# Kernel optimization log

Measured on AMD Instinct MI355X. Metric: run time of the kernel, lower is better.

Reference implementation:

```python
import jax, jax.numpy as jnp
import numpy as np

DIM = 512
HEADS = 8
DIM_HEAD = 64
LANDMARKS = 256
PINV_ITERS = 6
RES_K = 33


def layernorm(x, g, b, eps=1e-5):
    mu = jnp.mean(x, -1, keepdims=True)
    var = jnp.mean((x - mu) ** 2, -1, keepdims=True)
    return (x - mu) / jnp.sqrt(var + eps) * g + b


def moore_penrose_pinv(x, iters=PINV_ITERS):
    abs_x = jnp.abs(x)
    col = abs_x.sum(-1)
    row = abs_x.sum(-2)
    z = jnp.swapaxes(x, -1, -2) / (jnp.max(col) * jnp.max(row))
    I = jnp.eye(x.shape[-1], dtype=x.dtype)
    for _ in range(iters):
        xz = x @ z
        z = 0.25 * z @ (13.0 * I - xz @ (15.0 * I - xz @ (7.0 * I - xz)))
    return z


def nystrom_attention(x, Wqkv, Wout, bout, res_w):
    b, n, _ = x.shape
    m = LANDMARKS
    pad = (m - n % m) % m
    if pad:
        x = jnp.pad(x, ((0, 0), (pad, 0), (0, 0)))  # front pad, as in lucidrains impl
    qkv = x @ Wqkv  # (b, np, 3*inner)
    q, k, v = jnp.split(qkv, 3, axis=-1)
    to_heads = lambda t: t.reshape(b, -1, HEADS, DIM_HEAD).transpose(0, 2, 1, 3)
    q, k, v = to_heads(q), to_heads(k), to_heads(v)  # (b,h,np,d)
    q = q * (DIM_HEAD ** -0.5)
    l = -(-n // m)  # ceil(n/m), tokens per landmark
    ql = q.reshape(b, HEADS, m, l, DIM_HEAD).sum(3) / l  # (b,h,m,d)
    kl = k.reshape(b, HEADS, m, l, DIM_HEAD).sum(3) / l
    sim1 = jnp.einsum('bhid,bhjd->bhij', q, kl)   # (b,h,np,m)
    sim2 = jnp.einsum('bhid,bhjd->bhij', ql, kl)  # (b,h,m,m)
    sim3 = jnp.einsum('bhid,bhjd->bhij', ql, k)   # (b,h,m,np)
    a1 = jax.nn.softmax(sim1, -1)
    a2 = jax.nn.softmax(sim2, -1)
    a3 = jax.nn.softmax(sim3, -1)
    a2_inv = moore_penrose_pinv(a2)
    out = (a1 @ a2_inv) @ (a3 @ v)  # (b,h,np,d)
    # depthwise residual conv along sequence (kernel 33x1, groups=heads, no bias)
    res = jax.lax.conv_general_dilated(
        v, res_w, (1, 1), [(RES_K // 2, RES_K // 2), (0, 0)],
        dimension_numbers=('NCHW', 'OIHW', 'NCHW'), feature_group_count=HEADS)
    out = out + res
    out = out.transpose(0, 2, 1, 3).reshape(b, -1, HEADS * DIM_HEAD)
    out = out @ Wout + bout
    return out[:, -n:]


def depthwise2d(x, w, b, pad):
    y = jax.lax.conv_general_dilated(
        x, w, (1, 1), [(pad, pad), (pad, pad)],
        dimension_numbers=('NCHW', 'OIHW', 'NCHW'), feature_group_count=DIM)
    return y + b[None, :, None, None]


def ppeg(x, H, W, w7, b7, w5, b5, w3, b3):
    B, _, C = x.shape
    cls_tok, feat = x[:, :1], x[:, 1:]
    cnn = feat.transpose(0, 2, 1).reshape(B, C, H, W)
    y = depthwise2d(cnn, w7, b7, 3) + cnn + depthwise2d(cnn, w5, b5, 2) + depthwise2d(cnn, w3, b3, 1)
    y = y.reshape(B, C, H * W).transpose(0, 2, 1)
    return jnp.concatenate([cls_tok, y], axis=1)


def setup_inputs() -> dict:
    key = jax.random.key(0)
    ks = jax.random.split(key, 20)
    s = 0.02
    n_classes = 5
    inp = {
        'data': jax.random.normal(ks[0], (1, 15000, 1024), jnp.float32),
        'W_fc1': jax.random.normal(ks[1], (1024, DIM), jnp.float32) * s,
        'b_fc1': jnp.zeros((DIM,), jnp.float32),
        'cls_token': jax.random.normal(ks[2], (1, 1, DIM), jnp.float32),
        'ln1_g': jnp.ones((DIM,), jnp.float32), 'ln1_b': jnp.zeros((DIM,), jnp.float32),
        'qkv1': jax.random.normal(ks[3], (DIM, 3 * HEADS * DIM_HEAD), jnp.float32) * s,
        'out1_w': jax.random.normal(ks[4], (HEADS * DIM_HEAD, DIM), jnp.float32) * s,
        'out1_b': jnp.zeros((DIM,), jnp.float32),
        'res1': jax.random.normal(ks[5], (HEADS, 1, RES_K, 1), jnp.float32) * s,
        'w7': jax.random.normal(ks[6], (DIM, 1, 7, 7), jnp.float32) * s,
        'b7': jnp.zeros((DIM,), jnp.float32),
        'w5': jax.random.normal(ks[7], (DIM, 1, 5, 5), jnp.float32) * s,
        'b5': jnp.zeros((DIM,), jnp.float32),
        'w3': jax.random.normal(ks[8], (DIM, 1, 3, 3), jnp.float32) * s,
        'b3': jnp.zeros((DIM,), jnp.float32),
        'ln2_g': jnp.ones((DIM,), jnp.float32), 'ln2_b': jnp.zeros((DIM,), jnp.float32),
        'qkv2': jax.random.normal(ks[9], (DIM, 3 * HEADS * DIM_HEAD), jnp.float32) * s,
        'out2_w': jax.random.normal(ks[10], (HEADS * DIM_HEAD, DIM), jnp.float32) * s,
        'out2_b': jnp.zeros((DIM,), jnp.float32),
        'res2': jax.random.normal(ks[11], (HEADS, 1, RES_K, 1), jnp.float32) * s,
        'norm_g': jnp.ones((DIM,), jnp.float32), 'norm_b': jnp.zeros((DIM,), jnp.float32),
        'W_fc2': jax.random.normal(ks[12], (DIM, n_classes), jnp.float32) * s,
        'b_fc2': jnp.zeros((n_classes,), jnp.float32),
    }
    return inp


def reference(data, W_fc1, b_fc1, cls_token, ln1_g, ln1_b, qkv1, out1_w, out1_b, res1,
              w7, b7, w5, b5, w3, b3, ln2_g, ln2_b, qkv2, out2_w, out2_b, res2,
              norm_g, norm_b, W_fc2, b_fc2):
    h = jax.nn.relu(data @ W_fc1 + b_fc1)  # (B, N, 512)
    N = h.shape[1]
    _H = int(np.ceil(np.sqrt(N)))
    _W = _H
    add = _H * _W - N
    h = jnp.concatenate([h, h[:, :add]], axis=1)  # pad to square grid
    B = h.shape[0]
    h = jnp.concatenate([jnp.broadcast_to(cls_token, (B, 1, DIM)), h], axis=1)
    h = h + nystrom_attention(layernorm(h, ln1_g, ln1_b), qkv1, out1_w, out1_b, res1)
    h = ppeg(h, _H, _W, w7, b7, w5, b5, w3, b3)
    h = h + nystrom_attention(layernorm(h, ln2_g, ln2_b), qkv2, out2_w, out2_b, res2)
    h = layernorm(h, norm_g, norm_b)[:, 0]
    logits = h @ W_fc2 + b_fc2
    Y_prob = jax.nn.softmax(logits, -1)
    Y_hat = jnp.argmax(logits, -1)
    return logits, Y_prob, Y_hat
```

## Files before the change

kernel.cpp:

```cpp
#include <hip/hip_runtime.h>
#include <math.h>

#define NP 15360
#define NPQ 15488
#define NTOK 15130
#define HG 123

typedef __attribute__((ext_vector_type(8))) short s8b;
typedef __attribute__((ext_vector_type(4))) float f4;

__device__ inline float bf2f(ushort u) { return __uint_as_float(((unsigned)u) << 16); }
__device__ inline ushort f2bf(float f) {
    unsigned u = __float_as_uint(f);
    unsigned r = (u + 0x7fffu + ((u >> 16) & 1u)) >> 16;
    return (ushort)r;
}

__global__ __launch_bounds__(256)
void gemm_f32(const float* __restrict__ A, int lda, long sA,
              const float* __restrict__ B, int ldb, long sB,
              float* __restrict__ C, int ldc, long sC,
              int M, int N, int K,
              const float* __restrict__ bias,
              const float* __restrict__ E, int ldE, long sE, float eS,
              float cS, int relu, int accum)
{
    A += (long)blockIdx.z * sA;
    B += (long)blockIdx.z * sB;
    C += (long)blockIdx.z * sC;
    if (E) E += (long)blockIdx.z * sE;
    const int m0 = blockIdx.y * 64, n0 = blockIdx.x * 64;
    const int t = threadIdx.x;
    const int tx = t & 15, ty = t >> 4;
    __shared__ float As[16][64];
    __shared__ float Bs[16][64];
    float acc[4][4] = {};
    const int arow = t >> 2, akc = (t & 3) * 4;
    const int brow = t >> 4, bnc = (t & 15) * 4;
    for (int k0 = 0; k0 < K; k0 += 16) {
        float4 av = make_float4(0.f, 0.f, 0.f, 0.f);
        if (m0 + arow < M) av = *(const float4*)(A + (long)(m0 + arow) * lda + k0 + akc);
        As[akc + 0][arow] = av.x; As[akc + 1][arow] = av.y;
        As[akc + 2][arow] = av.z; As[akc + 3][arow] = av.w;
        float4 bv = *(const float4*)(B + (long)(k0 + brow) * ldb + n0 + bnc);
        *(float4*)&Bs[brow][bnc] = bv;
        __syncthreads();
#pragma unroll
        for (int kk = 0; kk < 16; ++kk) {
            float4 a4 = *(const float4*)&As[kk][ty * 4];
            float4 b4 = *(const float4*)&Bs[kk][tx * 4];
            float a[4] = {a4.x, a4.y, a4.z, a4.w};
            float b[4] = {b4.x, b4.y, b4.z, b4.w};
#pragma unroll
            for (int i = 0; i < 4; i++)
#pragma unroll
                for (int j = 0; j < 4; j++) acc[i][j] = fmaf(a[i], b[j], acc[i][j]);
        }
        __syncthreads();
    }
#pragma unroll
    for (int i = 0; i < 4; i++) {
        int m = m0 + ty * 4 + i;
        if (m < M) {
#pragma unroll
            for (int j = 0; j < 4; j++) {
                int n = n0 + tx * 4 + j;
                float v = cS * acc[i][j];
                if (E) v = fmaf(eS, E[(long)m * ldE + n], v);
                if (bias) v += bias[n];
                if (relu) v = fmaxf(v, 0.f);
                if (accum) C[(long)m * ldc + n] += v;
                else C[(long)m * ldc + n] = v;
            }
        }
    }
}

template<int MT, int NT, int WROWS, int WCOLS>
__global__ __launch_bounds__(256)
void gemm_mfma(const ushort* __restrict__ A, int lda, long sA,
               const ushort* __restrict__ Bt, int ldb, long sB,
               float* __restrict__ C, int ldc, long sC,
               int M, int K,
               const float* __restrict__ bias, int relu, int accum)
{
    constexpr int TM = MT * 16 * WROWS;
    constexpr int TN = NT * 16 * WCOLS;
    constexpr int BKP = 40;
    __shared__ ushort As[TM * BKP];
    __shared__ ushort Bs[TN * BKP];
    A  += (long)blockIdx.z * sA;
    Bt += (long)blockIdx.z * sB;
    C  += (long)blockIdx.z * sC;
    const int t = threadIdx.x;
    const int m0 = blockIdx.y * TM, n0 = blockIdx.x * TN;
    const int w = t >> 6, l = t & 63;
    const int wm = (w / WCOLS) * (MT * 16), wn = (w % WCOLS) * (NT * 16);
    const int lr = l & 15;
    const int lk = (l >> 4) * 8;
    f4 acc[MT][NT] = {};
    for (int k0 = 0; k0 < K; k0 += 32) {
        for (int c = t; c < TM * 4; c += 256) {
            int row = c >> 2, kc = (c & 3) * 8;
            s8b v = *(const s8b*)(A + (long)(m0 + row) * lda + k0 + kc);
            *(s8b*)(&As[row * BKP + kc]) = v;
        }
        for (int c = t; c < TN * 4; c += 256) {
            int row = c >> 2, kc = (c & 3) * 8;
            s8b v = *(const s8b*)(Bt + (long)(n0 + row) * ldb + k0 + kc);
            *(s8b*)(&Bs[row * BKP + kc]) = v;
        }
        __syncthreads();
        s8b af[MT], bf[NT];
#pragma unroll
        for (int i = 0; i < MT; i++) af[i] = *(const s8b*)(&As[(wm + i * 16 + lr) * BKP + lk]);
#pragma unroll
        for (int j = 0; j < NT; j++) bf[j] = *(const s8b*)(&Bs[(wn + j * 16 + lr) * BKP + lk]);
#pragma unroll
        for (int i = 0; i < MT; i++)
#pragma unroll
            for (int j = 0; j < NT; j++)
                acc[i][j] = __builtin_amdgcn_mfma_f32_16x16x32_bf16(af[i], bf[j], acc[i][j], 0, 0, 0);
        __syncthreads();
    }
    const int orow = (l >> 4) * 4;
#pragma unroll
    for (int i = 0; i < MT; i++) {
#pragma unroll
        for (int r = 0; r < 4; r++) {
            int m = m0 + wm + i * 16 + orow + r;
            if (m < M) {
#pragma unroll
                for (int j = 0; j < NT; j++) {
                    int n = n0 + wn + j * 16 + lr;
                    float vv = acc[i][j][r];
                    if (bias) vv += bias[n];
                    if (relu) vv = fmaxf(vv, 0.f);
                    if (accum) C[(long)m * ldc + n] += vv;
                    else C[(long)m * ldc + n] = vv;
                }
            }
        }
    }
}

__global__ __launch_bounds__(256)
void gemm_nn16(const ushort* __restrict__ A, const ushort* __restrict__ B,
               const ushort* __restrict__ E, ushort* __restrict__ C,
               int N, int K, float cS, float eS, long sAB)
{
    __shared__ ushort As[64 * 40];
    __shared__ ushort Bs[64 * 40];
    A += (long)blockIdx.z * sAB;
    B += (long)blockIdx.z * sAB;
    if (E) E += (long)blockIdx.z * sAB;
    C += (long)blockIdx.z * sAB;
    const int t = threadIdx.x;
    const int m0 = blockIdx.y * 64, n0 = blockIdx.x * 64;
    const int w = t >> 6, l = t & 63;
    const int wm = (w >> 1) * 32, wn = (w & 1) * 32;
    const int lr = l & 15, lk = (l >> 4) * 8;
    f4 acc[2][2] = {};
    for (int k0 = 0; k0 < K; k0 += 32) {
        {
            int row = t >> 2, kc = (t & 3) * 8;
            s8b v = *(const s8b*)(A + (long)(m0 + row) * K + k0 + kc);
            *(s8b*)(&As[row * 40 + kc]) = v;
            int kk = t >> 3, nc = (t & 7) * 8;
            s8b vb = *(const s8b*)(B + (long)(k0 + kk) * N + n0 + nc);
#pragma unroll
            for (int j = 0; j < 8; j++) Bs[(nc + j) * 40 + kk] = ((ushort*)&vb)[j];
        }
        __syncthreads();
        s8b af[2], bf[2];
#pragma unroll
        for (int i = 0; i < 2; i++) af[i] = *(const s8b*)(&As[(wm + i * 16 + lr) * 40 + lk]);
#pragma unroll
        for (int j = 0; j < 2; j++) bf[j] = *(const s8b*)(&Bs[(wn + j * 16 + lr) * 40 + lk]);
#pragma unroll
        for (int i = 0; i < 2; i++)
#pragma unroll
            for (int j = 0; j < 2; j++)
                acc[i][j] = __builtin_amdgcn_mfma_f32_16x16x32_bf16(af[i], bf[j], acc[i][j], 0, 0, 0);
        __syncthreads();
    }
    const int orow = (l >> 4) * 4;
#pragma unroll
    for (int i = 0; i < 2; i++)
#pragma unroll
        for (int r = 0; r < 4; r++) {
            int m = m0 + wm + i * 16 + orow + r;
#pragma unroll
            for (int j = 0; j < 2; j++) {
                int n = n0 + wn + j * 16 + lr;
                float vv = cS * acc[i][j][r];
                if (E) vv = fmaf(eS, bf2f(E[(long)m * N + n]), vv);
                C[(long)m * N + n] = f2bf(vv);
            }
        }
}

__global__ __launch_bounds__(256)
void gemm_qkv_mfma(const ushort* __restrict__ A, const ushort* __restrict__ Bt,
                   ushort* __restrict__ qo, ushort* __restrict__ ko, ushort* __restrict__ vo)
{
    constexpr int BKP = 40;
    __shared__ ushort As[128 * BKP];
    __shared__ ushort Bs[128 * BKP];
    const int t = threadIdx.x;
    const int m0 = blockIdx.y * 128, n0 = blockIdx.x * 128;
    const int w = t >> 6, l = t & 63;
    const int wm = (w >> 1) * 64, wn = (w & 1) * 64;
    const int lr = l & 15;
    const int lk = (l >> 4) * 8;
    f4 acc[4][4] = {};
    for (int k0 = 0; k0 < 512; k0 += 32) {
        for (int c = t; c < 512; c += 256) {
            int row = c >> 2, kc = (c & 3) * 8;
            s8b va = *(const s8b*)(A + (long)(m0 + row) * 512 + k0 + kc);
            *(s8b*)(&As[row * BKP + kc]) = va;
            s8b vb = *(const s8b*)(Bt + (long)(n0 + row) * 512 + k0 + kc);
            *(s8b*)(&Bs[row * BKP + kc]) = vb;
        }
        __syncthreads();
        s8b af[4], bf[4];
#pragma unroll
        for (int i = 0; i < 4; i++) af[i] = *(const s8b*)(&As[(wm + i * 16 + lr) * BKP + lk]);
#pragma unroll
        for (int j = 0; j < 4; j++) bf[j] = *(const s8b*)(&Bs[(wn + j * 16 + lr) * BKP + lk]);
#pragma unroll
        for (int i = 0; i < 4; i++)
#pragma unroll
            for (int j = 0; j < 4; j++)
                acc[i][j] = __builtin_amdgcn_mfma_f32_16x16x32_bf16(af[i], bf[j], acc[i][j], 0, 0, 0);
        __syncthreads();
    }
    const int orow = (l >> 4) * 4;
#pragma unroll
    for (int i = 0; i < 4; i++) {
#pragma unroll
        for (int r = 0; r < 4; r++) {
            int m = m0 + wm + i * 16 + orow + r;
#pragma unroll
            for (int j = 0; j < 4; j++) {
                int col = n0 + wn + j * 16 + lr;
                int which = col >> 9, h = (col >> 6) & 7, d = col & 63;
                float vv = acc[i][j][r];
                if (which == 0) vv *= 0.125f;
                ushort* dst = which == 0 ? qo : (which == 1 ? ko : vo);
                dst[((long)h * NPQ + m) * 64 + d] = f2bf(vv);
            }
        }
    }
}

__global__ __launch_bounds__(256)
void k_flash_a3v(const ushort* __restrict__ qlb, const ushort* __restrict__ kg,
                 const ushort* __restrict__ vg,
                 float* __restrict__ pacc, float* __restrict__ pml)
{
    const int c = blockIdx.x;
    const int qt = blockIdx.y;
    const int h = blockIdx.z;
    const int t = threadIdx.x;
    const int w = t >> 6, lane = t & 63;
    const int quad = lane >> 4, l16 = lane & 15;
    const s8b vones = {0x3F80, 0x3F80, 0x3F80, 0x3F80, 0x3F80, 0x3F80, 0x3F80, 0x3F80};

    __shared__ union {
        struct { ushort Vt[64][40]; ushort Ps[128][40]; } s;
        float Os[128][68];
    } L;

    s8b aq[2][2];
    const ushort* qbase = qlb + ((long)h * 256 + qt * 128 + w * 32) * 64;
#pragma unroll
    for (int mi = 0; mi < 2; mi++)
#pragma unroll
        for (int kf = 0; kf < 2; kf++)
            aq[mi][kf] = *(const s8b*)(qbase + (mi * 16 + l16) * 64 + kf * 32 + quad * 8);

    f4 oacc[2][4] = {};
    f4 lacc[2] = {};

    const ushort* kh = kg + (long)h * NPQ * 64;
    const ushort* vh = vg + (long)h * NPQ * 64;
    const int key0c = c * 256;

    for (int sub = 0; sub < 8; sub++) {
        int key0 = key0c + sub * 32;
        __syncthreads();
        {
            int kk = t >> 3 & 31;
            int dc = (t & 7) * 8;
            s8b vv = *(const s8b*)(vh + (long)(key0 + kk) * 64 + dc);
            int rot = (dc >> 3) & 3;
            int colp = (kk + rot * 8) & 31;
#pragma unroll
            for (int j = 0; j < 8; j++) L.s.Vt[dc + j][colp] = ((ushort*)&vv)[j];
        }
        s8b bq[2][2];
#pragma unroll
        for (int nj = 0; nj < 2; nj++)
#pragma unroll
            for (int kf = 0; kf < 2; kf++)
                bq[nj][kf] = *(const s8b*)(kh + (long)(key0 + nj * 16 + l16) * 64 + kf * 32 + quad * 8);
        f4 sacc[2][2] = {};
#pragma unroll
        for (int mi = 0; mi < 2; mi++)
#pragma unroll
            for (int nj = 0; nj < 2; nj++) {
                sacc[mi][nj] = __builtin_amdgcn_mfma_f32_16x16x32_bf16(aq[mi][0], bq[nj][0], sacc[mi][nj], 0, 0, 0);
                sacc[mi][nj] = __builtin_amdgcn_mfma_f32_16x16x32_bf16(aq[mi][1], bq[nj][1], sacc[mi][nj], 0, 0, 0);
            }
#pragma unroll
        for (int mi = 0; mi < 2; mi++)
#pragma unroll
            for (int r = 0; r < 4; r++) {
                int row = w * 32 + mi * 16 + quad * 4 + r;
                L.s.Ps[row][l16]      = f2bf(__expf(sacc[mi][0][r]));
                L.s.Ps[row][16 + l16] = f2bf(__expf(sacc[mi][1][r]));
            }
        __syncthreads();
        s8b ap[2], bv[4];
#pragma unroll
        for (int mi = 0; mi < 2; mi++)
            ap[mi] = *(const s8b*)(&L.s.Ps[w * 32 + mi * 16 + l16][quad * 8]);
#pragma unroll
        for (int dj = 0; dj < 4; dj++) {
            int d = dj * 16 + l16;
            int rot = (d >> 3) & 3;
            int cb = ((quad + rot) & 3) * 8;
            bv[dj] = *(const s8b*)(&L.s.Vt[d][cb]);
        }
#pragma unroll
        for (int mi = 0; mi < 2; mi++) {
#pragma unroll
            for (int dj = 0; dj < 4; dj++)
                oacc[mi][dj] = __builtin_amdgcn_mfma_f32_16x16x32_bf16(ap[mi], bv[dj], oacc[mi][dj], 0, 0, 0);
            lacc[mi] = __builtin_amdgcn_mfma_f32_16x16x32_bf16(ap[mi], vones, lacc[mi], 0, 0, 0);
        }
    }
    __syncthreads();
#pragma unroll
    for (int mi = 0; mi < 2; mi++)
#pragma unroll
        for (int dj = 0; dj < 4; dj++)
#pragma unroll
            for (int r = 0; r < 4; r++)
                L.Os[w * 32 + mi * 16 + quad * 4 + r][dj * 16 + l16] = oacc[mi][dj][r];
    long pbase = (long)(h * 60 + c);
    if (l16 == 0) {
#pragma unroll
        for (int mi = 0; mi < 2; mi++)
#pragma unroll
            for (int r = 0; r < 4; r++) {
                int i = qt * 128 + w * 32 + mi * 16 + quad * 4 + r;
                pml[pbase * 512 + i] = 0.f;
                pml[pbase * 512 + 256 + i] = lacc[mi][r];
            }
    }
    __syncthreads();
    float* pc = pacc + pbase * 16384 + qt * 128;
    int d = t >> 2, ig = t & 3;
#pragma unroll
    for (int u = 0; u < 8; u++) {
        int i0 = ig * 32 + u * 4;
        float4 v4 = make_float4(L.Os[i0][d], L.Os[i0 + 1][d], L.Os[i0 + 2][d], L.Os[i0 + 3][d]);
        *(float4*)(pc + (long)d * 256 + i0) = v4;
    }
}

__global__ __launch_bounds__(256)
void k_attn1(const ushort* __restrict__ qg, const ushort* __restrict__ klb,
             const ushort* __restrict__ BmT, const ushort* __restrict__ vg,
             const float* __restrict__ rw, ushort* __restrict__ ohb)
{
    const int m0 = blockIdx.x * 128;
    const int h = blockIdx.y;
    const int t = threadIdx.x;
    const int w = t >> 6, lane = t & 63;
    const int quad = lane >> 4, l16 = lane & 15;
    const s8b vones = {0x3F80, 0x3F80, 0x3F80, 0x3F80, 0x3F80, 0x3F80, 0x3F80, 0x3F80};

    __shared__ union {
        ushort Ps[2][128][40];
        ushort Os[128][68];
    } L;
    __shared__ __attribute__((aligned(16))) ushort Vs[160][64];

    const ushort* vh = vg + (long)h * NPQ * 64;
    {
        const ushort* srcw = vh + (long)(214 + m0 + w * 40) * 64 + lane * 8;
        ushort* dstw = &Vs[w * 40][0];
#pragma unroll
        for (int it = 0; it < 5; it++)
            __builtin_amdgcn_global_load_lds(
                (const __attribute__((address_space(1))) void*)(srcw + it * 512),
                (__attribute__((address_space(3))) void*)(dstw + it * 512),
                16, 0, 0);
    }

    s8b aq[2][2];
    const ushort* qbase = qg + ((long)h * NPQ + 230 + m0 + w * 32) * 64;
#pragma unroll
    for (int mi = 0; mi < 2; mi++)
#pragma unroll
        for (int kf = 0; kf < 2; kf++)
            aq[mi][kf] = *(const s8b*)(qbase + (mi * 16 + l16) * 64 + kf * 32 + quad * 8);

    const ushort* kh = klb + (long)h * 16384;
    const ushort* bmt = BmT + (long)h * 16384;

    f4 oacc[2][4] = {};
    f4 lacc[2] = {};
#pragma unroll
    for (int sub = 0; sub < 8; sub++) {
        int key0 = sub * 32;
        s8b bq[2][2], bv[4];
#pragma unroll
        for (int nj = 0; nj < 2; nj++)
#pragma unroll
            for (int kf = 0; kf < 2; kf++)
                bq[nj][kf] = *(const s8b*)(kh + (long)(key0 + nj * 16 + l16) * 64 + kf * 32 + quad * 8);
#pragma unroll
        for (int dj = 0; dj < 4; dj++)
            bv[dj] = *(const s8b*)(bmt + (long)(dj * 16 + l16) * 256 + key0 + quad * 8);
        f4 sacc[2][2] = {};
#pragma unroll
        for (int mi = 0; mi < 2; mi++)
#pragma unroll
            for (int nj = 0; nj < 2; nj++) {
                sacc[mi][nj] = __builtin_amdgcn_mfma_f32_16x16x32_bf16(aq[mi][0], bq[nj][0], sacc[mi][nj], 0, 0, 0);
                sacc[mi][nj] = __builtin_amdgcn_mfma_f32_16x16x32_bf16(aq[mi][1], bq[nj][1], sacc[mi][nj], 0, 0, 0);
            }
        int par = sub & 1;
#pragma unroll
        for (int mi = 0; mi < 2; mi++)
#pragma unroll
            for (int r = 0; r < 4; r++) {
                int row = w * 32 + mi * 16 + quad * 4 + r;
                L.Ps[par][row][l16]      = f2bf(__expf(sacc[mi][0][r]));
                L.Ps[par][row][16 + l16] = f2bf(__expf(sacc[mi][1][r]));
            }
        s8b ap[2];
#pragma unroll
        for (int mi = 0; mi < 2; mi++)
            ap[mi] = *(const s8b*)(&L.Ps[par][w * 32 + mi * 16 + l16][quad * 8]);
#pragma unroll
        for (int mi = 0; mi < 2; mi++) {
#pragma unroll
            for (int dj = 0; dj < 4; dj++)
                oacc[mi][dj] = __builtin_amdgcn_mfma_f32_16x16x32_bf16(ap[mi], bv[dj], oacc[mi][dj], 0, 0, 0);
            lacc[mi] = __builtin_amdgcn_mfma_f32_16x16x32_bf16(ap[mi], vones, lacc[mi], 0, 0, 0);
        }
    }
    __syncthreads();

    if (214 + m0 + 160 > NP) {
        for (int r = w * 32; r < w * 32 + 64 && r < 160; ++r)
            if (214 + m0 + r >= NP) Vs[r][lane] = 0;
    }

#pragma unroll
    for (int mi = 0; mi < 2; mi++)
#pragma unroll
        for (int r = 0; r < 4; r++) {
            float inv = 1.f / lacc[mi][r];
            int row = w * 32 + mi * 16 + quad * 4 + r;
#pragma unroll
            for (int dj = 0; dj < 4; dj++)
                L.Os[row][dj * 16 + l16] = f2bf(oacc[mi][dj][r] * inv);
        }
    float rwf[33];
#pragma unroll
    for (int kk = 0; kk < 33; kk++) rwf[kk] = rw[h * 33 + kk];
#pragma unroll
    for (int half = 0; half < 2; half++) {
        const int rbase = w * 32 + half * 16;
        float conv[16];
#pragma unroll
        for (int i = 0; i < 16; i++) conv[i] = 0.f;
#pragma unroll
        for (int s = 0; s < 48; s++) {
            float val = bf2f(Vs[rbase + s][lane]);
#pragma unroll
            for (int i = 0; i < 16; i++) {
                int kk = s - i;
                if (kk >= 0 && kk < 33) conv[i] = fmaf(rwf[kk], val, conv[i]);
            }
        }
        int t0 = m0 + rbase;
#pragma unroll
        for (int i = 0; i < 16; i++) {
            int tk = t0 + i;
            if (tk < NTOK) {
                float val = bf2f(L.Os[rbase + i][lane]) + conv[i];
                ohb[(long)tk * 512 + h * 64 + lane] = f2bf(val);
            }
        }
    }
}

__global__ __launch_bounds__(256)
void k_layernorm(const float* __restrict__ h, ushort* __restrict__ xln,
                 const float* __restrict__ g, const float* __restrict__ b, int pad)
{
    int row = blockIdx.x, t = threadIdx.x;
    if (row < pad) {
        xln[(long)row * 512 + t] = 0;
        xln[(long)row * 512 + t + 256] = 0;
        return;
    }
    const float* src = h + (long)(row - pad) * 512;
    float x1 = src[t], x2 = src[t + 256];
    float s = x1 + x2, q = x1 * x1 + x2 * x2;
    __shared__ float rs[4], rq[4], st[2];
    int wid = t >> 6, lane = t & 63;
#pragma unroll
    for (int o = 32; o > 0; o >>= 1) { s += __shfl_down(s, o); q += __shfl_down(q, o); }
    if (lane == 0) { rs[wid] = s; rq[wid] = q; }
    __syncthreads();
    if (t == 0) {
        float S = rs[0] + rs[1] + rs[2] + rs[3];
        float Q = rq[0] + rq[1] + rq[2] + rq[3];
        float mean = S / 512.f;
        float var = Q / 512.f - mean * mean;
        st[0] = mean; st[1] = rsqrtf(var + 1e-5f);
    }
    __syncthreads();
    float mean = st[0], rstd = st[1];
    xln[(long)row * 512 + t] = f2bf((x1 - mean) * rstd * g[t] + b[t]);
    xln[(long)row * 512 + t + 256] = f2bf((x2 - mean) * rstd * g[t + 256] + b[t + 256]);
}

__global__ __launch_bounds__(256)
void k_padcls(float* __restrict__ hbuf, const float* __restrict__ cls)
{
    int i = blockIdx.x, t = threadIdx.x;
    if (i == 0) { hbuf[t] = cls[t]; hbuf[t + 256] = cls[t + 256]; }
    else {
        hbuf[(long)(15000 + i) * 512 + t] = hbuf[(long)i * 512 + t];
        hbuf[(long)(15000 + i) * 512 + t + 256] = hbuf[(long)i * 512 + t + 256];
    }
}

__global__ __launch_bounds__(256)
void k_wT(const float* __restrict__ Wm, ushort* __restrict__ Wt, int K, int N, long sW, long sWt)
{
    Wm += (long)blockIdx.z * sW; Wt += (long)blockIdx.z * sWt;
    __shared__ float tile[32][33];
    int tx = threadIdx.x & 31, ty = threadIdx.x >> 5;
    int n0 = blockIdx.x * 32, k0 = blockIdx.y * 32;
#pragma unroll
    for (int u = 0; u < 4; u++) tile[ty + u * 8][tx] = Wm[(long)(k0 + ty + u * 8) * N + n0 + tx];
    __syncthreads();
#pragma unroll
    for (int u = 0; u < 4; u++) Wt[(long)(n0 + ty + u * 8) * K + k0 + tx] = f2bf(tile[tx][ty + u * 8]);
}

__global__ __launch_bounds__(256)
void k_cvt(const float4* __restrict__ src, ushort4* __restrict__ dst, long n4)
{
    long i = (long)blockIdx.x * 256 + threadIdx.x;
    if (i < n4) {
        float4 v = src[i];
        ushort4 o;
        o.x = f2bf(v.x); o.y = f2bf(v.y); o.z = f2bf(v.z); o.w = f2bf(v.w);
        dst[i] = o;
    }
}

__global__ __launch_bounds__(256)
void k_b2f(const ushort4* __restrict__ src, float4* __restrict__ dst, long n4)
{
    long i = (long)blockIdx.x * 256 + threadIdx.x;
    if (i < n4) {
        ushort4 v = src[i];
        dst[i] = make_float4(bf2f(v.x), bf2f(v.y), bf2f(v.z), bf2f(v.w));
    }
}

__global__ __launch_bounds__(64)
void k_landmarks(const ushort* __restrict__ q, const ushort* __restrict__ k,
                 float* __restrict__ ql, ushort* __restrict__ qlb,
                 float* __restrict__ klT, ushort* __restrict__ klb,
                 unsigned* __restrict__ scal)
{
    int i = blockIdx.x, h = blockIdx.y, d = threadIdx.x;
    if (i == 0 && h == 0 && d == 0) { scal[0] = 0u; scal[1] = 0u; }
    long base = ((long)h * NPQ + (long)i * 60) * 64 + d;
    float sq = 0.f, sk = 0.f;
    for (int j = 0; j < 60; j++) { sq += bf2f(q[base + j * 64]); sk += bf2f(k[base + j * 64]); }
    float qv = sq / 60.f, kv = sk / 60.f;
    ql[((long)h * 256 + i) * 64 + d] = qv;
    qlb[((long)h * 256 + i) * 64 + d] = f2bf(qv);
    klT[((long)h * 64 + d) * 256 + i] = kv;
    klb[((long)h * 256 + i) * 64 + d] = f2bf(kv);
}

__global__ __launch_bounds__(256)
void k_softmax256(float* __restrict__ X, ushort* __restrict__ X16, long headStride)
{
    float* row = X + (long)blockIdx.y * headStride + (long)blockIdx.x * 256;
    int t = threadIdx.x, wid = t >> 6, lane = t & 63;
    float x = row[t];
    __shared__ float rm[4], rsum[4], fin[2];
    float m = x;
#pragma unroll
    for (int o = 32; o > 0; o >>= 1) m = fmaxf(m, __shfl_down(m, o));
    if (lane == 0) rm[wid] = m;
    __syncthreads();
    if (t == 0) fin[0] = fmaxf(fmaxf(rm[0], rm[1]), fmaxf(rm[2], rm[3]));
    __syncthreads();
    float e = __expf(x - fin[0]);
    float s = e;
#pragma unroll
    for (int o = 32; o > 0; o >>= 1) s += __shfl_down(s, o);
    if (lane == 0) rsum[wid] = s;
    __syncthreads();
    if (t == 0) fin[1] = rsum[0] + rsum[1] + rsum[2] + rsum[3];
    __syncthreads();
    float v = e / fin[1];
    row[t] = v;
    if (X16) X16[(long)blockIdx.y * headStride + (long)blockIdx.x * 256 + t] = f2bf(v);
}

__global__ __launch_bounds__(256)
void k_colmax(const float* __restrict__ a2, unsigned* __restrict__ scal)
{
    int h = blockIdx.x, t = threadIdx.x, wid = t >> 6, lane = t & 63;
    const float* A = a2 + (long)h * 65536;
    float cs = 0.f, rs = 0.f;
    for (int i = 0; i < 256; i++) cs += A[(long)i * 256 + t];
    for (int j = 0; j < 256; j++) rs += A[(long)t * 256 + j];
    __shared__ float r1[4], r2[4];
    float m1v = cs, m2v = rs;
#pragma unroll
    for (int o = 32; o > 0; o >>= 1) {
        m1v = fmaxf(m1v, __shfl_down(m1v, o));
        m2v = fmaxf(m2v, __shfl_down(m2v, o));
    }
    if (lane == 0) { r1[wid] = m1v; r2[wid] = m2v; }
    __syncthreads();
    if (t == 0) {
        float a = fmaxf(fmaxf(r1[0], r1[1]), fmaxf(r1[2], r1[3]));
        float b = fmaxf(fmaxf(r2[0], r2[1]), fmaxf(r2[2], r2[3]));
        atomicMax(scal + 0, __float_as_uint(a));
        atomicMax(scal + 1, __float_as_uint(b));
    }
}

__global__ __launch_bounds__(256)
void k_zinit(const float* __restrict__ a2, ushort* __restrict__ zb, const unsigned* __restrict__ scal)
{
    float s = 1.f / (__uint_as_float(scal[0]) * __uint_as_float(scal[1]));
    const float* A = a2 + (long)blockIdx.z * 65536;
    ushort* Z = zb + (long)blockIdx.z * 65536;
    __shared__ float tile[32][33];
    int tx = threadIdx.x & 31, ty = threadIdx.x >> 5;
    int i0 = blockIdx.x * 32, j0 = blockIdx.y * 32;
#pragma unroll
    for (int u = 0; u < 4; u++) tile[ty + u * 8][tx] = A[(long)(j0 + ty + u * 8) * 256 + i0 + tx];
    __syncthreads();
#pragma unroll
    for (int u = 0; u < 4; u++) Z[(long)(i0 + ty + u * 8) * 256 + j0 + tx] = f2bf(tile[tx][ty + u * 8] * s);
}

__global__ __launch_bounds__(256)
void k_a3v_merge(const float* __restrict__ pacc, const float* __restrict__ pml,
                 float* __restrict__ t1)
{
    int d = blockIdx.x, h = blockIdx.y, i = threadIdx.x;
    float M = -INFINITY, L = 0.f, num = 0.f;
    for (int c = 0; c < 60; c++) {
        float mc = pml[(long)(h * 60 + c) * 2 * 256 + i];
        float lc = pml[((long)(h * 60 + c) * 2 + 1) * 256 + i];
        float ac = pacc[((long)(h * 60 + c) * 64 + d) * 256 + i];
        if (mc > M) {
            float f = __expf(M - mc);
            num = num * f + ac; L = L * f + lc; M = mc;
        } else {
            float p = __expf(mc - M);
            num = fmaf(p, ac, num); L = fmaf(p, lc, L);
        }
    }
    t1[((long)h * 256 + i) * 64 + d] = num / L;
}

__global__ __launch_bounds__(256)
void k_cls(const ushort* __restrict__ qb, const float* __restrict__ klT,
           const float* __restrict__ Bm, const ushort* __restrict__ vb,
           const float* __restrict__ rw, float* __restrict__ oh)
{
    int h = blockIdx.x, t = threadIdx.x, wid = t >> 6, lane = t & 63;
    __shared__ float qs[64], p[256], red[256];
    __shared__ float rm[4], rsum[4], fin[2];
    if (t < 64) qs[t] = bf2f(qb[((long)h * NPQ + 230) * 64 + t]);
    __syncthreads();
    float s = 0.f;
    for (int d = 0; d < 64; d++) s = fmaf(qs[d], klT[((long)h * 64 + d) * 256 + t], s);
    float m = s;
#pragma unroll
    for (int o = 32; o > 0; o >>= 1) m = fmaxf(m, __shfl_down(m, o));
    if (lane == 0) rm[wid] = m;
    __syncthreads();
    if (t == 0) fin[0] = fmaxf(fmaxf(rm[0], rm[1]), fmaxf(rm[2], rm[3]));
    __syncthreads();
    float e = __expf(s - fin[0]);
    float ss = e;
#pragma unroll
    for (int o = 32; o > 0; o >>= 1) ss += __shfl_down(ss, o);
    if (lane == 0) rsum[wid] = ss;
    __syncthreads();
    if (t == 0) fin[1] = rsum[0] + rsum[1] + rsum[2] + rsum[3];
    __syncthreads();
    p[t] = e / fin[1];
    __syncthreads();
    int d = t & 63, grp = t >> 6;
    float o = 0.f;
    for (int j = grp * 64; j < grp * 64 + 64; j++) o = fmaf(p[j], Bm[((long)h * 256 + j) * 64 + d], o);
    red[t] = o;
    __syncthreads();
    if (t < 64) {
        float val = red[t] + red[t + 64] + red[t + 128] + red[t + 192];
#pragma unroll
        for (int kk = 0; kk < 33; kk++)
            val = fmaf(rw[h * 33 + kk], bf2f(vb[((long)h * NPQ + 214 + kk) * 64 + t]), val);
        oh[h * 64 + t] = val;
    }
}

__global__ __launch_bounds__(256)
void k_copy4(const float4* __restrict__ src, float4* __restrict__ dst, long n4)
{
    long i = (long)blockIdx.x * 256 + threadIdx.x;
    if (i < n4) dst[i] = src[i];
}

__global__ __launch_bounds__(512)
void k_wcomb(const float* __restrict__ w7, const float* __restrict__ b7,
             const float* __restrict__ w5, const float* __restrict__ b5,
             const float* __restrict__ w3, const float* __restrict__ b3,
             float* __restrict__ wc, float* __restrict__ bc)
{
    int k = blockIdx.x, c = threadIdx.x;
    int kr = k / 7, kc = k % 7;
    float v = w7[c * 49 + k];
    if (kr >= 1 && kr <= 5 && kc >= 1 && kc <= 5) v += w5[c * 25 + (kr - 1) * 5 + (kc - 1)];
    if (kr >= 2 && kr <= 4 && kc >= 2 && kc <= 4) v += w3[c * 9 + (kr - 2) * 3 + (kc - 2)];
    if (k == 24) v += 1.f;
    wc[k * 512 + c] = v;
    if (k == 0) bc[c] = b7[c] + b5[c] + b3[c];
}

__global__ __launch_bounds__(256)
void k_ppeg2(const float* __restrict__ cnn, float* __restrict__ hbuf,
             const float* __restrict__ wc, const float* __restrict__ bc)
{
    __shared__ ushort tile[140][64];
    int t = threadIdx.x;
    int cp = t & 31;
    int g = t >> 5;
    int c0 = blockIdx.x * 8, r0 = blockIdx.y * 4, cb = blockIdx.z * 64;
    for (int idx = t; idx < 140 * 32; idx += 256) {
        int pos = idx >> 5, pp = idx & 31;
        int pr = pos / 14, pc = pos % 14;
        int gr = r0 + pr - 3, gc = c0 + pc - 3;
        float v0 = 0.f, v1 = 0.f;
        if (gr >= 0 && gr < HG && gc >= 0 && gc < HG) {
            const float* src = cnn + (long)(gr * HG + gc) * 512 + cb + pp * 2;
            v0 = src[0]; v1 = src[1];
        }
        tile[pos][pp * 2] = f2bf(v0);
        tile[pos][pp * 2 + 1] = f2bf(v1);
    }
    __syncthreads();
    float acc[4][2] = {};
    for (int kr = 0; kr < 7; kr++)
#pragma unroll
        for (int kc = 0; kc < 7; kc++) {
            float w0 = wc[(kr * 7 + kc) * 512 + cb + cp * 2];
            float w1 = wc[(kr * 7 + kc) * 512 + cb + cp * 2 + 1];
#pragma unroll
            for (int u = 0; u < 4; u++) {
                int p = g * 4 + u;
                int orow = p >> 3, ocol = p & 7;
                unsigned pk = *(const unsigned*)&tile[(orow + kr) * 14 + (ocol + kc)][cp * 2];
                acc[u][0] = fmaf(w0, bf2f((ushort)pk), acc[u][0]);
                acc[u][1] = fmaf(w1, bf2f((ushort)(pk >> 16)), acc[u][1]);
            }
        }
    float b0 = bc[cb + cp * 2], b1 = bc[cb + cp * 2 + 1];
#pragma unroll
    for (int u = 0; u < 4; u++) {
        int p = g * 4 + u;
        int orow = p >> 3, ocol = p & 7;
        int gr = r0 + orow, gc = c0 + ocol;
        if (gr < HG && gc < HG) {
            float* dst = hbuf + (long)(1 + gr * HG + gc) * 512 + cb + cp * 2;
            dst[0] = acc[u][0] + b0;
            dst[1] = acc[u][1] + b1;
        }
    }
}

__global__ __launch_bounds__(256)
void k_final(const float* __restrict__ hbuf, const float* __restrict__ g,
             const float* __restrict__ b, const float* __restrict__ W2,
             const float* __restrict__ b2, float* __restrict__ out)
{
    __shared__ float y[512];
    __shared__ float rs[4], rq[4], st[2], lg[8];
    int t = threadIdx.x, wid = t >> 6, lane = t & 63;
    float x1 = hbuf[t], x2 = hbuf[t + 256];
    float s = x1 + x2, q = x1 * x1 + x2 * x2;
#pragma unroll
    for (int o = 32; o > 0; o >>= 1) { s += __shfl_down(s, o); q += __shfl_down(q, o); }
    if (lane == 0) { rs[wid] = s; rq[wid] = q; }
    __syncthreads();
    if (t == 0) {
        float S = rs[0] + rs[1] + rs[2] + rs[3];
        float Q = rq[0] + rq[1] + rq[2] + rq[3];
        float mean = S / 512.f;
        float var = Q / 512.f - mean * mean;
        st[0] = mean; st[1] = rsqrtf(var + 1e-5f);
    }
    __syncthreads();
    float mean = st[0], rstd = st[1];
    y[t] = (x1 - mean) * rstd * g[t] + b[t];
    y[t + 256] = (x2 - mean) * rstd * g[t + 256] + b[t + 256];
    __syncthreads();
    if (t < 5) {
        float acc = b2[t];
        for (int kx = 0; kx < 512; kx++) acc = fmaf(y[kx], W2[kx * 5 + t], acc);
        lg[t] = acc;
    }
    __syncthreads();
    if (t == 0) {
        float mx = lg[0]; int am = 0;
        for (int j = 1; j < 5; j++) if (lg[j] > mx) { mx = lg[j]; am = j; }
        float e[5], se = 0.f;
        for (int j = 0; j < 5; j++) { e[j] = __expf(lg[j] - mx); se += e[j]; }
        for (int j = 0; j < 5; j++) { out[j] = lg[j]; out[5 + j] = e[j] / se; }
        out[10] = (float)am;
    }
}

extern "C" void kernel_launch(void* const* d_in, const int* in_sizes, int n_in,
                              void* d_out, int out_size, void* d_ws, size_t ws_size,
                              hipStream_t stream)
{
    const float* data  = (const float*)d_in[0];
    const float* Wfc1  = (const float*)d_in[1];
    const float* bfc1  = (const float*)d_in[2];
    const float* cls   = (const float*)d_in[3];
    const float* ln1g  = (const float*)d_in[4];
    const float* ln1b  = (const float*)d_in[5];
    const float* qkv1  = (const float*)d_in[6];
    const float* out1w = (const float*)d_in[7];
    const float* out1b = (const float*)d_in[8];
    const float* res1  = (const float*)d_in[9];
    const float* w7    = (const float*)d_in[10];
    const float* b7    = (const float*)d_in[11];
    const float* w5    = (const float*)d_in[12];
    const float* b5    = (const float*)d_in[13];
    const float* w3    = (const float*)d_in[14];
    const float* b3    = (const float*)d_in[15];
    const float* ln2g  = (const float*)d_in[16];
    const float* ln2b  = (const float*)d_in[17];
    const float* qkv2  = (const float*)d_in[18];
    const float* out2w = (const float*)d_in[19];
    const float* out2b = (const float*)d_in[20];
    const float* res2  = (const float*)d_in[21];
    const float* normg = (const float*)d_in[22];
    const float* normb = (const float*)d_in[23];
    const float* Wfc2  = (const float*)d_in[24];
    const float* bfc2  = (const float*)d_in[25];
    float* out = (float*)d_out;

    float* W = (float*)d_ws;
    size_t off = 0;
    auto alloc = [&](size_t n) { size_t o = off; off += (n + 255) & ~(size_t)255; return o; };
    float*  hbuf   = W + alloc((size_t)NTOK * 512);
    float*  ohreg  = W + alloc((size_t)15232 * 512);
    float*  oh     = ohreg;
    ushort* xln    = (ushort*)ohreg;
    ushort* qb16   = (ushort*)(W + alloc((size_t)8 * NPQ * 32));
    ushort* kb16   = (ushort*)(W + alloc((size_t)8 * NPQ * 32));
    ushort* vb16   = (ushort*)(W + alloc((size_t)8 * NPQ * 32));
    float*  ql     = W + alloc(8 * 256 * 64);
    ushort* qlb    = (ushort*)(W + alloc(8 * 256 * 32));
    float*  klT    = W + alloc(8 * 64 * 256);
    ushort* klb    = (ushort*)(W + alloc(8 * 256 * 32));
    float*  a2     = W + alloc(8 * 65536);
    ushort* a2b    = (ushort*)(W + alloc(8 * 32768));
    ushort* zb0    = (ushort*)(W + alloc(8 * 32768));
    ushort* zb1    = (ushort*)(W + alloc(8 * 32768));
    ushort* m1b    = (ushort*)(W + alloc(8 * 32768));
    ushort* mab    = (ushort*)(W + alloc(8 * 32768));
    ushort* mbb    = (ushort*)(W + alloc(8 * 32768));
    float*  z0     = W + alloc(8 * 65536);
    float*  t1     = W + alloc(8 * 256 * 64);
    float*  Bm     = W + alloc(8 * 256 * 64);
    ushort* BmbT   = (ushort*)(W + alloc(8 * 256 * 32));
    float*  scal   = W + alloc(64);
    ushort* ohb16  = (ushort*)(W + alloc((size_t)15232 * 256));
    ushort* WfcT   = (ushort*)(W + alloc(1024 * 256));
    ushort* qkv1T  = (ushort*)(W + alloc(1536 * 256));
    ushort* qkv2T  = (ushort*)(W + alloc(1536 * 256));
    ushort* out1T  = (ushort*)(W + alloc(512 * 256));
    ushort* out2T  = (ushort*)(W + alloc(512 * 256));
    float*  wc     = W + alloc(49 * 512);
    float*  bc     = W + alloc(512);
    float*  big    = W + alloc(8110080);
    ushort* datab  = (ushort*)big;
    float*  pacc   = big;
    float*  pml    = big + 7864320;
    float*  cnn    = big;
    if (ws_size < off * sizeof(float)) return;

    k_wT<<<dim3(16, 32, 1), 256, 0, stream>>>(Wfc1, WfcT, 1024, 512, 0, 0);
    k_wT<<<dim3(48, 16, 1), 256, 0, stream>>>(qkv1, qkv1T, 512, 1536, 0, 0);
    k_wT<<<dim3(48, 16, 1), 256, 0, stream>>>(qkv2, qkv2T, 512, 1536, 0, 0);
    k_wT<<<dim3(16, 16, 1), 256, 0, stream>>>(out1w, out1T, 512, 512, 0, 0);
    k_wT<<<dim3(16, 16, 1), 256, 0, stream>>>(out2w, out2T, 512, 512, 0, 0);
    k_wcomb<<<49, 512, 0, stream>>>(w7, b7, w5, b5, w3, b3, wc, bc);
    k_cvt<<<15000, 256, 0, stream>>>((const float4*)data, (ushort4*)datab, 3840000);
    gemm_mfma<4, 4, 2, 2><<<dim3(4, 118, 1), 256, 0, stream>>>(
        datab, 1024, 0, WfcT, 1024, 0, hbuf + 512, 512, 0, 15000, 1024, bfc1, 1, 0);
    k_padcls<<<130, 256, 0, stream>>>(hbuf, cls);

    auto layer = [&](const float* lng, const float* lnb, const ushort* qkvT,
                     const float* outW, const ushort* outT, const float* outB,
                     const float* resW, bool full) {
        k_layernorm<<<NP, 256, 0, stream>>>(hbuf, xln, lng, lnb, 230);
        gemm_qkv_mfma<<<dim3(12, 120, 1), 256, 0, stream>>>(xln, qkvT, qb16, kb16, vb16);
        k_landmarks<<<dim3(256, 8), 64, 0, stream>>>(qb16, kb16, ql, qlb, klT, klb, (unsigned*)scal);
        gemm_f32<<<dim3(4, 4, 8), 256, 0, stream>>>(ql, 64, 16384, klT, 256, 16384,
            a2, 256, 65536, 256, 256, 64, nullptr, nullptr, 0, 0, 0.f, 1.f, 0, 0);
        k_softmax256<<<dim3(256, 8), 256, 0, stream>>>(a2, a2b, 65536);
        k_colmax<<<8, 256, 0, stream>>>(a2, (unsigned*)scal);
        k_zinit<<<dim3(8, 8, 8), 256, 0, stream>>>(a2, zb0, (const unsigned*)scal);
        ushort* zbi = zb0; ushort* zbo = zb1;
        for (int it = 0; it < 6; ++it) {
            gemm_nn16<<<dim3(4, 4, 8), 256, 0, stream>>>(a2b, zbi, nullptr, m1b, 256, 256, 1.f, 0.f, 65536);
            gemm_nn16<<<dim3(4, 4, 8), 256, 0, stream>>>(m1b, m1b, m1b, mab, 256, 256, -1.f, 7.f, 65536);
            gemm_nn16<<<dim3(4, 4, 8), 256, 0, stream>>>(m1b, mab, m1b, mbb, 256, 256, -1.f, 15.f, 65536);
            gemm_nn16<<<dim3(4, 4, 8), 256, 0, stream>>>(zbi, mbb, zbi, zbo, 256, 256, -0.25f, 3.25f, 65536);
            ushort* tmp = zbi; zbi = zbo; zbo = tmp;
        }
        k_b2f<<<512, 256, 0, stream>>>((const ushort4*)zbi, (float4*)z0, 131072);
        k_flash_a3v<<<dim3(60, 2, 8), 256, 0, stream>>>(qlb, kb16, vb16, pacc, pml);
        k_a3v_merge<<<dim3(64, 8), 256, 0, stream>>>(pacc, pml, t1);
        gemm_f32<<<dim3(1, 4, 8), 256, 0, stream>>>(z0, 256, 65536, t1, 64, 16384,
            Bm, 64, 16384, 256, 64, 256, nullptr, nullptr, 0, 0, 0.f, 1.f, 0, 0);
        if (full) {
            k_wT<<<dim3(2, 8, 8), 256, 0, stream>>>(Bm, BmbT, 256, 64, 16384, 16384);
            k_attn1<<<dim3(119, 8), 256, 0, stream>>>(qb16, klb, BmbT, vb16, resW, ohb16);
            gemm_mfma<4, 4, 2, 2><<<dim3(4, 119, 1), 256, 0, stream>>>(
                ohb16, 512, 0, outT, 512, 0, hbuf, 512, 0, NTOK, 512, outB, 0, 1);
        } else {
            k_cls<<<8, 256, 0, stream>>>(qb16, klT, Bm, vb16, resW, oh);
            gemm_f32<<<dim3(8, 1, 1), 256, 0, stream>>>(oh, 512, 0, outW, 512, 0,
                hbuf, 512, 0, 1, 512, 512, outB, nullptr, 0, 0, 0.f, 1.f, 0, 1);
        }
    };

    layer(ln1g, ln1b, qkv1T, out1w, out1T, out1b, res1, true);
    k_copy4<<<(1936512 + 255) / 256, 256, 0, stream>>>((const float4*)(hbuf + 512), (float4*)cnn, 1936512);
    k_ppeg2<<<dim3(16, 31, 8), 256, 0, stream>>>(cnn, hbuf, wc, bc);
    layer(ln2g, ln2b, qkv2T, out2w, out2T, out2b, res2, false);
    k_final<<<1, 256, 0, stream>>>(hbuf, normg, normb, Wfc2, bfc2, out);
}
```

Baseline: 1.264 ms.

## Rework PPEG depthwise conv tiling with register sliding window and fp32 tile

The fused 7x7 depthwise PPEG conv now uses a 8x16 output tile per block with 32 channels, keeping the shared tile in fp32 loaded with float4. Each thread caches 14 input columns per kernel row in registers and computes 8 horizontally adjacent outputs, so every LDS value is reused across the 7 kernel columns. This removes the bf16 rounding and the per-tap LDS reads, and cuts the halo overhead per output. The cost is higher register use and a different grid shape.

```diff
diff --git a/kernel.cpp b/kernel.cpp
--- a/kernel.cpp
+++ b/kernel.cpp
@@ -755,52 +755,60 @@
 }
 
 __global__ __launch_bounds__(256)
-void k_ppeg2(const float* __restrict__ cnn, float* __restrict__ hbuf,
+void k_ppeg3(const float* __restrict__ cnn, float* __restrict__ hbuf,
              const float* __restrict__ wc, const float* __restrict__ bc)
 {
-    __shared__ ushort tile[140][64];
-    int t = threadIdx.x;
-    int cp = t & 31;
-    int g = t >> 5;
-    int c0 = blockIdx.x * 8, r0 = blockIdx.y * 4, cb = blockIdx.z * 64;
-    for (int idx = t; idx < 140 * 32; idx += 256) {
-        int pos = idx >> 5, pp = idx & 31;
-        int pr = pos / 14, pc = pos % 14;
+    __shared__ float tile[14 * 22][32];
+    const int t = threadIdx.x;
+    const int c0 = blockIdx.x * 16;
+    const int r0 = blockIdx.y * 8;
+    const int cb = blockIdx.z * 32;
+    for (int idx = t; idx < 308 * 8; idx += 256) {
+        int pos = idx >> 3, c4 = (idx & 7) * 4;
+        int pr = pos / 22, pc = pos - pr * 22;
         int gr = r0 + pr - 3, gc = c0 + pc - 3;
-        float v0 = 0.f, v1 = 0.f;
-        if (gr >= 0 && gr < HG && gc >= 0 && gc < HG) {
-            const float* src = cnn + (long)(gr * HG + gc) * 512 + cb + pp * 2;
-            v0 = src[0]; v1 = src[1];
-        }
-        tile[pos][pp * 2] = f2bf(v0);
-        tile[pos][pp * 2 + 1] = f2bf(v1);
-    }
-    __syncthreads();
-    float acc[4][2] = {};
-    for (int kr = 0; kr < 7; kr++)
+        float4 v = make_float4(0.f, 0.f, 0.f, 0.f);
+        if (gr >= 0 && gr < HG && gc >= 0 && gc < HG)
+            v = *(const float4*)(cnn + (long)(gr * HG + gc) * 512 + cb + c4);
+        *(float4*)&tile[pos][c4] = v;
+    }
+    __syncthreads();
+    const int cp = t & 15;
+    const int slot = t >> 4;
+    const int orow = slot >> 1;
+    const int ohalf = (slot & 1) * 8;
+    float a0[8], a1[8];
+#pragma unroll
+    for (int i = 0; i < 8; i++) { a0[i] = 0.f; a1[i] = 0.f; }
+    for (int kr = 0; kr < 7; kr++) {
+        float w0[14], w1[14];
+        const float* trow = &tile[(orow + kr) * 22 + ohalf][cp * 2];
+#pragma unroll
+        for (int j = 0; j < 14; j++) {
+            float2 v = *(const float2*)(trow + j * 32);
+            w0[j] = v.x; w1[j] = v.y;
+        }
 #pragma unroll
         for (int kc = 0; kc < 7; kc++) {
-            float w0 = wc[(kr * 7 + kc) * 512 + cb + cp * 2];
-            float w1 = wc[(kr * 7 + kc) * 512 + cb + cp * 2 + 1];
-#pragma unroll
-            for (int u = 0; u < 4; u++) {
-                int p = g * 4 + u;
-                int orow = p >> 3, ocol = p & 7;
-                unsigned pk = *(const unsigned*)&tile[(orow + kr) * 14 + (ocol + kc)][cp * 2];
-                acc[u][0] = fmaf(w0, bf2f((ushort)pk), acc[u][0]);
-                acc[u][1] = fmaf(w1, bf2f((ushort)(pk >> 16)), acc[u][1]);
-            }
-        }
-    float b0 = bc[cb + cp * 2], b1 = bc[cb + cp * 2 + 1];
-#pragma unroll
-    for (int u = 0; u < 4; u++) {
-        int p = g * 4 + u;
-        int orow = p >> 3, ocol = p & 7;
-        int gr = r0 + orow, gc = c0 + ocol;
-        if (gr < HG && gc < HG) {
-            float* dst = hbuf + (long)(1 + gr * HG + gc) * 512 + cb + cp * 2;
-            dst[0] = acc[u][0] + b0;
-            dst[1] = acc[u][1] + b1;
+            float2 wv = *(const float2*)(wc + (long)(kr * 7 + kc) * 512 + cb + cp * 2);
+#pragma unroll
+            for (int i = 0; i < 8; i++) {
+                a0[i] = fmaf(wv.x, w0[i + kc], a0[i]);
+                a1[i] = fmaf(wv.y, w1[i + kc], a1[i]);
+            }
+        }
+    }
+    const float2 bv = *(const float2*)(bc + cb + cp * 2);
+    const int gr = r0 + orow;
+    if (gr < HG) {
+#pragma unroll
+        for (int i = 0; i < 8; i++) {
+            int gc = c0 + ohalf + i;
+            if (gc < HG) {
+                float* dst = hbuf + (long)(1 + gr * HG + gc) * 512 + cb + cp * 2;
+                dst[0] = a0[i] + bv.x;
+                dst[1] = a1[i] + bv.y;
+            }
         }
     }
 }
@@ -969,7 +977,7 @@
 
     layer(ln1g, ln1b, qkv1T, out1w, out1T, out1b, res1, true);
     k_copy4<<<(1936512 + 255) / 256, 256, 0, stream>>>((const float4*)(hbuf + 512), (float4*)cnn, 1936512);
-    k_ppeg2<<<dim3(16, 31, 8), 256, 0, stream>>>(cnn, hbuf, wc, bc);
+    k_ppeg3<<<dim3(8, 16, 16), 256, 0, stream>>>(cnn, hbuf, wc, bc);
     layer(ln2g, ln2b, qkv2T, out2w, out2T, out2b, res2, false);
     k_final<<<1, 256, 0, stream>>>(hbuf, normg, normb, Wfc2, bfc2, out);
 }
```

Result: no change. 1.273 ms (+0.8%).
